# Kernel tuning notes

Hardware: AMD Instinct MI355X
Metric: run time of the kernel (lower is better)

## Reference

```python
import jax, jax.numpy as jnp
import numpy as np

EPS = 1e-12  # torch F.normalize eps


def setup_inputs() -> dict:
    key = jax.random.key(0)
    k1, k2, k3, k4, k5 = jax.random.split(key, 5)
    N, C, H, W = 32, 512, 32, 32
    E = 1024   # expansion * dim
    G = 8      # group
    D = E // G # 128, per-group channel dim
    K = 64     # num_clusters
    x = jax.random.normal(k1, (N, C, H, W), dtype=jnp.float32)
    W1 = jax.random.normal(k2, (E, C), dtype=jnp.float32) / np.sqrt(C)
    W2 = jax.random.normal(k3, (G, E), dtype=jnp.float32) / np.sqrt(E)
    Wc = jax.random.normal(k4, (K, D), dtype=jnp.float32) / np.sqrt(D)
    centroids = jax.random.uniform(k5, (K, D), dtype=jnp.float32)
    return {"x": x, "W1": W1, "W2": W2, "Wc": Wc, "centroids": centroids}


def reference(x, W1, W2, Wc, centroids):
    # x: [N, C, H, W]; W1: [E, C]; W2: [G, E]; Wc: [K, D]; centroids: [K, D]
    N, C, H, W = x.shape
    E = W1.shape[0]
    G = W2.shape[0]
    K, D = Wc.shape
    P = H * W
    # descriptor-wise L2 normalization over channel dim
    norm = jnp.linalg.norm(x, axis=1, keepdims=True)
    x = x / jnp.maximum(norm, EPS)
    # linear1 on channels: [N, E, P]
    xe = jnp.einsum('ncp,ec->nep', x.reshape(N, C, P), W1)
    # grouped features: [N, G, D, P]
    xg = xe.reshape(N, G, D, P)
    # attention gate: sigmoid(linear2)  -> [N, G, P]
    att = jax.nn.sigmoid(jnp.einsum('nep,ge->ngp', xe, W2))
    # 1x1 conv = per-pixel matmul with cluster weights -> [N, G, K, P]
    soft_assign = jax.nn.softmax(jnp.einsum('ngdp,kd->ngkp', xg, Wc), axis=2)
    # combined per-(cluster,pixel) weight
    w = soft_assign * att[:, :, None, :]  # [N, G, K, P]
    # NetVLAD residual aggregation, algebraically decomposed to avoid the
    # giant [N,G,K,D,P] intermediate:
    #   vlad[n,k,d] = sum_{g,p} w * xg  -  centroids[k,d] * sum_{g,p} w
    agg = jnp.einsum('ngkp,ngdp->nkd', w, xg)  # [N, K, D]
    wsum = w.sum(axis=(1, 3))                  # [N, K]
    vlad = agg - wsum[:, :, None] * centroids[None]  # [N, K, D]
    return vlad.reshape(N, K * D)
```

## Files before the change

kernel.cpp:

```cpp
#include <hip/hip_runtime.h>


#define N_  32
#define C_  512
#define P_  1024
#define E_  1024
#define G_  8
#define D_  128
#define K_  64

typedef __attribute__((ext_vector_type(8))) short bf16x8;
typedef __attribute__((ext_vector_type(4))) float f32x4;

__device__ __forceinline__ unsigned short f2b(float f) {
    union { float f; unsigned u; } v; v.f = f;
    unsigned r = (v.u + 0x7FFFu + ((v.u >> 16) & 1u)) >> 16;
    return (unsigned short)r;
}
__device__ __forceinline__ float b2f(unsigned short h) {
    union { unsigned u; float f; } v; v.u = ((unsigned)h) << 16;
    return v.f;
}

__device__ __forceinline__ void gl_lds16(const void* g, void* l) {
    __builtin_amdgcn_global_load_lds(
        (const __attribute__((address_space(1))) void*)g,
        (__attribute__((address_space(3))) void*)l, 16, 0, 0);
}

__global__ __launch_bounds__(256) void k0_prep(const float* __restrict__ W1,
                                               const float* __restrict__ Wc,
                                               unsigned short* __restrict__ W1b,
                                               unsigned short* __restrict__ Vb) {
    int bid = blockIdx.x;
    int t = threadIdx.x;
    int i0 = bid * 512 + t;
    W1b[i0]       = f2b(W1[i0]);
    W1b[i0 + 256] = f2b(W1[i0 + 256]);
    int ch = bid & 1, k = (bid >> 1) & 63, g = bid >> 7;
    int c = ch * 256 + t;
    float acc = 0.f;
    #pragma unroll 8
    for (int d = 0; d < 128; ++d)
        acc += Wc[k * 128 + d] * W1[(g * 128 + d) * C_ + c];
    Vb[(g * 64 + k) * C_ + c] = f2b(acc);
}

__global__ __launch_bounds__(256) void k1_norm_transpose(const float* __restrict__ x,
                                                         unsigned short* __restrict__ xhat_t) {
    __shared__ short xc[128 * 256];
    __shared__ float red[256];
    __shared__ float rn[64];
    int n = blockIdx.y;
    int p0 = blockIdx.x * 64;
    int t = threadIdx.x;
    int ps = t & 63, cs = t >> 6;

    float ss = 0.f;
    for (int i = 0; i < 128; ++i) {
        float v = x[((size_t)(n * C_ + cs * 128 + i)) * P_ + p0 + ps];
        ss += v * v;
        xc[i * 256 + t] = (short)f2b(v);
    }
    red[t] = ss;
    __syncthreads();
    if (t < 64) {
        float s = red[t] + red[64 + t] + red[128 + t] + red[192 + t];
        rn[t] = 1.0f / fmaxf(sqrtf(s), 1e-12f);
    }
    __syncthreads();

    float r = rn[ps];
    size_t base = ((size_t)(n * P_ + p0 + ps)) * C_ + cs * 128;
    #pragma unroll
    for (int jj = 0; jj < 16; ++jj) {
        bf16x8 o;
        #pragma unroll
        for (int j = 0; j < 8; ++j)
            o[j] = (short)f2b(b2f((unsigned short)xc[(jj * 8 + j) * 256 + t]) * r);
        *(bf16x8*)&xhat_t[base + jj * 8] = o;
    }
}

__global__ __launch_bounds__(256) void k2_gemm_xe(const unsigned short* __restrict__ W1b,
                                                  const unsigned short* __restrict__ xhat_t,
                                                  unsigned short* __restrict__ xe) {
    __shared__ __align__(16) short As[128 * 64];
    __shared__ __align__(16) short Bs[128 * 64];
    int n = blockIdx.y;
    int e0 = (blockIdx.x >> 3) * 128;
    int p0 = (blockIdx.x & 7) * 128;
    int t = threadIdx.x;
    int w = t >> 6, l = t & 63, q = l >> 4, l15 = l & 15;
    int wr = w >> 1, wc = w & 1;

    f32x4 acc[4][4];
    #pragma unroll
    for (int mi = 0; mi < 4; ++mi)
        #pragma unroll
        for (int ni = 0; ni < 4; ++ni)
            acc[mi][ni] = (f32x4){0.f, 0.f, 0.f, 0.f};

    for (int ks = 0; ks < 8; ++ks) {
        int k0 = ks * 64;
        #pragma unroll
        for (int i = 0; i < 4; ++i) {
            int ch = i * 256 + t;
            int row = ch >> 3, c8 = ch & 7;
            gl_lds16(&W1b[(e0 + row) * C_ + k0 + ((c8 ^ (row & 7)) * 8)], &As[ch * 8]);
        }
        #pragma unroll
        for (int i = 0; i < 4; ++i) {
            int ch = i * 256 + t;
            int row = ch >> 3, c8 = ch & 7;
            gl_lds16(&xhat_t[((size_t)(n * P_ + p0 + row)) * C_ + k0 + ((c8 ^ (row & 7)) * 8)], &Bs[ch * 8]);
        }
        __syncthreads();

        #pragma unroll
        for (int kk = 0; kk < 2; ++kk) {
            bf16x8 af[4], bf[4];
            #pragma unroll
            for (int mi = 0; mi < 4; ++mi)
                af[mi] = *(const bf16x8*)&As[(wr * 64 + mi * 16 + l15) * 64 + (((kk * 4 + q) ^ (l15 & 7)) * 8)];
            #pragma unroll
            for (int ni = 0; ni < 4; ++ni)
                bf[ni] = *(const bf16x8*)&Bs[(wc * 64 + ni * 16 + l15) * 64 + (((kk * 4 + q) ^ (l15 & 7)) * 8)];
            #pragma unroll
            for (int mi = 0; mi < 4; ++mi)
                #pragma unroll
                for (int ni = 0; ni < 4; ++ni)
                    acc[mi][ni] = __builtin_amdgcn_mfma_f32_16x16x32_bf16(af[mi], bf[ni], acc[mi][ni], 0, 0, 0);
        }
        __syncthreads();
    }

    #pragma unroll
    for (int mi = 0; mi < 4; ++mi) {
        #pragma unroll
        for (int ni = 0; ni < 4; ++ni) {
            #pragma unroll
            for (int r = 0; r < 4; ++r) {
                int e = e0 + wr * 64 + mi * 16 + q * 4 + r;
                int p = p0 + wc * 64 + ni * 16 + l15;
                xe[((size_t)(n * E_ + e)) * P_ + p] = f2b(acc[mi][ni][r]);
            }
        }
    }
}

__global__ __launch_bounds__(256) void k3a_att_part(const unsigned short* __restrict__ xe,
                                                    const float* __restrict__ W2,
                                                    float* __restrict__ att_part) {
    int n = blockIdx.y;
    int ec = blockIdx.x;
    int t = threadIdx.x;
    int e0 = ec * 64;
    f32x4 acc[8];
    #pragma unroll
    for (int g = 0; g < 8; ++g) acc[g] = (f32x4){0.f, 0.f, 0.f, 0.f};
    #pragma unroll 4
    for (int i = 0; i < 64; ++i) {
        int e = e0 + i;
        ushort4 v4 = *(const ushort4*)&xe[((size_t)(n * E_ + e)) * P_ + t * 4];
        f32x4 vf = {b2f(v4.x), b2f(v4.y), b2f(v4.z), b2f(v4.w)};
        #pragma unroll
        for (int g = 0; g < 8; ++g)
            acc[g] += vf * W2[g * E_ + e];
    }
    #pragma unroll
    for (int g = 0; g < 8; ++g)
        *(f32x4*)&att_part[(((size_t)(n * 16 + ec)) * 8 + g) * P_ + t * 4] = acc[g];
}

__global__ __launch_bounds__(256) void k3b_att_reduce(const float* __restrict__ att_part,
                                                      float* __restrict__ att_s) {
    int idx = blockIdx.x * 256 + threadIdx.x;
    int p = idx & 1023;
    int g = (idx >> 10) & 7;
    int n = idx >> 13;
    float s = 0.f;
    #pragma unroll
    for (int ec = 0; ec < 16; ++ec)
        s += att_part[(((size_t)(n * 16 + ec)) * 8 + g) * P_ + p];
    att_s[idx] = 1.0f / (1.0f + __expf(-s));
}

__global__ __launch_bounds__(256) void k4_assign_agg(const unsigned short* __restrict__ Vb,
                                                     const unsigned short* __restrict__ xhat_t,
                                                     const unsigned short* __restrict__ xe,
                                                     const float* __restrict__ att_s,
                                                     float* __restrict__ agg_part,
                                                     float* __restrict__ wsum_part) {
    __shared__ __align__(16) char smem[8192 + 16384 + 34816 + 17408];
    short* As2   = (short*)smem;
    short* Bs2   = (short*)(smem + 8192);
    short* xglds = (short*)(smem + 24576);
    short* wlds  = (short*)(smem + 59392);

    int b = blockIdx.y * 16 + blockIdx.x;
    int work = (b & 7) * 64 + (b >> 3);
    int n = work >> 4, g = work & 7, ph = (work >> 3) & 1;

    int t = threadIdx.x;
    int w = t >> 6, l = t & 63, q = l >> 4, l15 = l & 15;

    f32x4 acc_a[4][2];
    #pragma unroll
    for (int mi = 0; mi < 4; ++mi)
        #pragma unroll
        for (int ni = 0; ni < 2; ++ni)
            acc_a[mi][ni] = (f32x4){0.f, 0.f, 0.f, 0.f};
    float wsp[16];
    #pragma unroll
    for (int j = 0; j < 16; ++j) wsp[j] = 0.f;

    for (int cc = 0; cc < 4; ++cc) {
        int p0c = ph * 512 + cc * 128;

        #pragma unroll
        for (int i = 0; i < 8; ++i) {
            int ch = i * 256 + t;
            int row = ch / 17, col = (ch % 17) * 8;
            gl_lds16(&xe[((size_t)(n * E_ + g * 128 + row)) * P_ + p0c + col], &xglds[ch * 8]);
        }
        if (t < 128) {
            int ch = 2048 + t;
            int row = ch / 17, col = (ch % 17) * 8;
            gl_lds16(&xe[((size_t)(n * E_ + g * 128 + row)) * P_ + p0c + col], &xglds[ch * 8]);
        }

        f32x4 acc_s[4][2];
        #pragma unroll
        for (int mi = 0; mi < 4; ++mi)
            #pragma unroll
            for (int ni = 0; ni < 2; ++ni)
                acc_s[mi][ni] = (f32x4){0.f, 0.f, 0.f, 0.f};

        for (int ks = 0; ks < 8; ++ks) {
            int k0 = ks * 64;
            #pragma unroll
            for (int i = 0; i < 2; ++i) {
                int ch = i * 256 + t;
                int row = ch >> 3, c8 = ch & 7;
                gl_lds16(&Vb[(g * 64 + row) * C_ + k0 + ((c8 ^ (row & 7)) * 8)], &As2[ch * 8]);
            }
            #pragma unroll
            for (int i = 0; i < 4; ++i) {
                int ch = i * 256 + t;
                int row = ch >> 3, c8 = ch & 7;
                gl_lds16(&xhat_t[((size_t)(n * P_ + p0c + row)) * C_ + k0 + ((c8 ^ (row & 7)) * 8)], &Bs2[ch * 8]);
            }
            __syncthreads();
            #pragma unroll
            for (int kk = 0; kk < 2; ++kk) {
                bf16x8 af[4], bf2[2];
                #pragma unroll
                for (int mi = 0; mi < 4; ++mi)
                    af[mi] = *(const bf16x8*)&As2[(mi * 16 + l15) * 64 + (((kk * 4 + q) ^ (l15 & 7)) * 8)];
                #pragma unroll
                for (int ni = 0; ni < 2; ++ni)
                    bf2[ni] = *(const bf16x8*)&Bs2[(w * 32 + ni * 16 + l15) * 64 + (((kk * 4 + q) ^ (l15 & 7)) * 8)];
                #pragma unroll
                for (int mi = 0; mi < 4; ++mi)
                    #pragma unroll
                    for (int ni = 0; ni < 2; ++ni)
                        acc_s[mi][ni] = __builtin_amdgcn_mfma_f32_16x16x32_bf16(af[mi], bf2[ni], acc_s[mi][ni], 0, 0, 0);
            }
            __syncthreads();
        }

        #pragma unroll
        for (int ni = 0; ni < 2; ++ni) {
            float m = -1e30f;
            #pragma unroll
            for (int mi = 0; mi < 4; ++mi)
                #pragma unroll
                for (int r = 0; r < 4; ++r)
                    m = fmaxf(m, acc_s[mi][ni][r]);
            m = fmaxf(m, __shfl_xor(m, 16));
            m = fmaxf(m, __shfl_xor(m, 32));
            float s = 0.f;
            #pragma unroll
            for (int mi = 0; mi < 4; ++mi)
                #pragma unroll
                for (int r = 0; r < 4; ++r) {
                    float e = __expf(acc_s[mi][ni][r] - m);
                    acc_s[mi][ni][r] = e;
                    s += e;
                }
            s += __shfl_xor(s, 16);
            s += __shfl_xor(s, 32);

            int pcol = p0c + w * 32 + ni * 16 + l15;
            float av = att_s[(((size_t)(n * G_ + g)) * P_) + pcol];
            float scale = av / s;

            #pragma unroll
            for (int mi = 0; mi < 4; ++mi)
                #pragma unroll
                for (int r = 0; r < 4; ++r) {
                    float wv = acc_s[mi][ni][r] * scale;
                    wsp[mi * 4 + r] += wv;
                    wlds[(mi * 16 + q * 4 + r) * 136 + (w * 32 + ni * 16 + l15)] = (short)f2b(wv);
                }
        }
        __syncthreads();

        #pragma unroll
        for (int pk = 0; pk < 4; ++pk) {
            bf16x8 a2[4], b2[2];
            #pragma unroll
            for (int mi = 0; mi < 4; ++mi)
                a2[mi] = *(const bf16x8*)&wlds[(mi * 16 + l15) * 136 + pk * 32 + q * 8];
            #pragma unroll
            for (int ni = 0; ni < 2; ++ni)
                b2[ni] = *(const bf16x8*)&xglds[(w * 32 + ni * 16 + l15) * 136 + pk * 32 + q * 8];
            #pragma unroll
            for (int mi = 0; mi < 4; ++mi)
                #pragma unroll
                for (int ni = 0; ni < 2; ++ni)
                    acc_a[mi][ni] = __builtin_amdgcn_mfma_f32_16x16x32_bf16(a2[mi], b2[ni], acc_a[mi][ni], 0, 0, 0);
        }
        __syncthreads();
    }

    size_t base = (((size_t)(n * G_ + g)) * 2 + ph) * 64;
    #pragma unroll
    for (int mi = 0; mi < 4; ++mi)
        #pragma unroll
        for (int ni = 0; ni < 2; ++ni)
            #pragma unroll
            for (int r = 0; r < 4; ++r) {
                int k = mi * 16 + q * 4 + r;
                int d = w * 32 + ni * 16 + l15;
                agg_part[(base + k) * 128 + d] = acc_a[mi][ni][r];
            }

    #pragma unroll
    for (int j = 0; j < 16; ++j) {
        float v = wsp[j];
        v += __shfl_xor(v, 1);
        v += __shfl_xor(v, 2);
        v += __shfl_xor(v, 4);
        v += __shfl_xor(v, 8);
        if (l15 == 0) {
            int k = (j >> 2) * 16 + q * 4 + (j & 3);
            wsum_part[((((size_t)(n * G_ + g)) * 2 + ph) * 4 + w) * 64 + k] = v;
        }
    }
}

__global__ __launch_bounds__(256) void k5_final(const float* __restrict__ agg_part,
                                                const float* __restrict__ wsum_part,
                                                const float* __restrict__ centroids,
                                                float* __restrict__ out) {
    int idx = blockIdx.x * 256 + threadIdx.x;
    int d = idx & 127;
    int k = (idx >> 7) & 63;
    int n = idx >> 13;
    float ws = 0.f;
    #pragma unroll
    for (int g = 0; g < 8; ++g)
        #pragma unroll
        for (int ph = 0; ph < 2; ++ph)
            #pragma unroll
            for (int w2 = 0; w2 < 4; ++w2)
                ws += wsum_part[((((size_t)(n * G_ + g)) * 2 + ph) * 4 + w2) * 64 + k];
    float agg = 0.f;
    #pragma unroll
    for (int g = 0; g < 8; ++g)
        #pragma unroll
        for (int ph = 0; ph < 2; ++ph)
            agg += agg_part[(((((size_t)(n * G_ + g)) * 2 + ph) * 64) + k) * 128 + d];
    out[idx] = agg - ws * centroids[k * 128 + d];
}

extern "C" void kernel_launch(void* const* d_in, const int* in_sizes, int n_in,
                              void* d_out, int out_size, void* d_ws, size_t ws_size,
                              hipStream_t stream) {
    const float* x         = (const float*)d_in[0];
    const float* W1        = (const float*)d_in[1];
    const float* W2        = (const float*)d_in[2];
    const float* Wc        = (const float*)d_in[3];
    const float* centroids = (const float*)d_in[4];
    float* out = (float*)d_out;

    char* ws = (char*)d_ws;
    unsigned short* W1b      = (unsigned short*)(ws + 0);
    unsigned short* Vb       = (unsigned short*)(ws + 1048576);
    unsigned short* xhat_t   = (unsigned short*)(ws + 1572864);
    unsigned short* xe       = (unsigned short*)(ws + 35127296);
    float*          att_s    = (float*)(ws + 102236160);
    float*          att_part = (float*)(ws + 103284736);
    float*          agg_part = (float*)(ws + 103284736);
    float*          wsum_part= (float*)(ws + 120061952);

    hipLaunchKernelGGL(k0_prep,        dim3(1024), dim3(256), 0, stream, W1, Wc, W1b, Vb);
    hipLaunchKernelGGL(k1_norm_transpose, dim3(16, 32), dim3(256), 0, stream, x, xhat_t);
    hipLaunchKernelGGL(k2_gemm_xe,     dim3(64, 32), dim3(256), 0, stream, W1b, xhat_t, xe);
    hipLaunchKernelGGL(k3a_att_part,   dim3(16, 32), dim3(256), 0, stream, xe, W2, att_part);
    hipLaunchKernelGGL(k3b_att_reduce, dim3(1024), dim3(256), 0, stream, att_part, att_s);
    hipLaunchKernelGGL(k4_assign_agg,  dim3(16, 32), dim3(256), 0, stream, Vb, xhat_t, xe,
                       att_s, agg_part, wsum_part);
    hipLaunchKernelGGL(k5_final,       dim3(1024), dim3(256), 0, stream,
                       agg_part, wsum_part, centroids, out);
}
```

Measured before the change: 242.7 us.

## Double-buffer assignment GEMM in k4 with register A-fragments and manual waitcnt pipeline

Rewrites the k4 soft-assignment GEMM loop as a fully unrolled double-buffered pipeline. The xhat tiles alternate between two LDS buffers, the Vb fragments are loaded straight into registers instead of staged through LDS, and explicit vmcnt waits with sched barriers overlap the next loads with the current MFMAs. The xg tile load moves to the end of the pipeline and uses an XOR-swizzled 128-wide layout instead of padding, and the LDS for the w tile now aliases the B buffers. The attention values are prefetched early. The hand-set waitcnt counts and buffer aliasing are fragile and raise register pressure.

```diff
diff --git a/kernel.cpp b/kernel.cpp
--- a/kernel.cpp
+++ b/kernel.cpp
@@ -27,6 +27,9 @@
         (const __attribute__((address_space(1))) void*)g,
         (__attribute__((address_space(3))) void*)l, 16, 0, 0);
 }
+
+#define SB  __builtin_amdgcn_sched_barrier(0)
+#define BAR __builtin_amdgcn_s_barrier()
 
 __global__ __launch_bounds__(256) void k0_prep(const float* __restrict__ W1,
                                                const float* __restrict__ Wc,
@@ -186,17 +189,67 @@
     att_s[idx] = 1.0f / (1.0f + __expf(-s));
 }
 
+__device__ __forceinline__ void load_af(bf16x8* dst, const unsigned short* __restrict__ Vb,
+                                        int g, int ks, int l15, int q) {
+    #pragma unroll
+    for (int mi = 0; mi < 4; ++mi)
+        #pragma unroll
+        for (int kk = 0; kk < 2; ++kk)
+            dst[mi * 2 + kk] = *(const bf16x8*)&Vb[(size_t)((g * 64 + mi * 16 + l15) * C_)
+                                                  + ks * 64 + kk * 32 + q * 8];
+}
+
+__device__ __forceinline__ void stage_b(short* buf, const unsigned short* __restrict__ xhat_t,
+                                        int n, int p0c, int k0, int t) {
+    #pragma unroll
+    for (int i = 0; i < 4; ++i) {
+        int ch = i * 256 + t;
+        int row = ch >> 3, c8 = ch & 7;
+        gl_lds16(&xhat_t[((size_t)(n * P_ + p0c + row)) * C_ + k0 + ((c8 ^ (row & 7)) * 8)],
+                 &buf[ch * 8]);
+    }
+}
+
+__device__ __forceinline__ void stage_xg(short* xglds, const unsigned short* __restrict__ xe,
+                                         int n, int g, int p0c, int t) {
+    #pragma unroll
+    for (int i = 0; i < 8; ++i) {
+        int ch = i * 256 + t;
+        int row = ch >> 4, c16 = ch & 15;
+        gl_lds16(&xe[((size_t)(n * E_ + g * 128 + row)) * P_ + p0c + ((c16 ^ (row & 7)) * 8)],
+                 &xglds[ch * 8]);
+    }
+}
+
+__device__ __forceinline__ void mfma_s(f32x4 acc[4][2], const short* buf, const bf16x8* af,
+                                       int w, int q, int l15) {
+    #pragma unroll
+    for (int kk = 0; kk < 2; ++kk) {
+        bf16x8 b[2];
+        #pragma unroll
+        for (int ni = 0; ni < 2; ++ni)
+            b[ni] = *(const bf16x8*)&buf[(w * 32 + ni * 16 + l15) * 64
+                                         + (((kk * 4 + q) ^ (l15 & 7)) * 8)];
+        #pragma unroll
+        for (int mi = 0; mi < 4; ++mi)
+            #pragma unroll
+            for (int ni = 0; ni < 2; ++ni)
+                acc[mi][ni] = __builtin_amdgcn_mfma_f32_16x16x32_bf16(
+                    af[mi * 2 + kk], b[ni], acc[mi][ni], 0, 0, 0);
+    }
+}
+
 __global__ __launch_bounds__(256) void k4_assign_agg(const unsigned short* __restrict__ Vb,
                                                      const unsigned short* __restrict__ xhat_t,
                                                      const unsigned short* __restrict__ xe,
                                                      const float* __restrict__ att_s,
                                                      float* __restrict__ agg_part,
                                                      float* __restrict__ wsum_part) {
-    __shared__ __align__(16) char smem[8192 + 16384 + 34816 + 17408];
-    short* As2   = (short*)smem;
-    short* Bs2   = (short*)(smem + 8192);
-    short* xglds = (short*)(smem + 24576);
-    short* wlds  = (short*)(smem + 59392);
+    __shared__ __align__(16) char smem[65536];
+    short* Bs0   = (short*)smem;
+    short* Bs1   = (short*)(smem + 16384);
+    short* xglds = (short*)(smem + 32768);
+    short* wlds  = (short*)smem;
 
     int b = blockIdx.y * 16 + blockIdx.x;
     int work = (b & 7) * 64 + (b >> 3);
@@ -215,21 +268,10 @@
     #pragma unroll
     for (int j = 0; j < 16; ++j) wsp[j] = 0.f;
 
+    #pragma unroll 1
     for (int cc = 0; cc < 4; ++cc) {
         int p0c = ph * 512 + cc * 128;
 
-        #pragma unroll
-        for (int i = 0; i < 8; ++i) {
-            int ch = i * 256 + t;
-            int row = ch / 17, col = (ch % 17) * 8;
-            gl_lds16(&xe[((size_t)(n * E_ + g * 128 + row)) * P_ + p0c + col], &xglds[ch * 8]);
-        }
-        if (t < 128) {
-            int ch = 2048 + t;
-            int row = ch / 17, col = (ch % 17) * 8;
-            gl_lds16(&xe[((size_t)(n * E_ + g * 128 + row)) * P_ + p0c + col], &xglds[ch * 8]);
-        }
-
         f32x4 acc_s[4][2];
         #pragma unroll
         for (int mi = 0; mi < 4; ++mi)
@@ -237,38 +279,45 @@
             for (int ni = 0; ni < 2; ++ni)
                 acc_s[mi][ni] = (f32x4){0.f, 0.f, 0.f, 0.f};
 
-        for (int ks = 0; ks < 8; ++ks) {
-            int k0 = ks * 64;
-            #pragma unroll
-            for (int i = 0; i < 2; ++i) {
-                int ch = i * 256 + t;
-                int row = ch >> 3, c8 = ch & 7;
-                gl_lds16(&Vb[(g * 64 + row) * C_ + k0 + ((c8 ^ (row & 7)) * 8)], &As2[ch * 8]);
-            }
-            #pragma unroll
-            for (int i = 0; i < 4; ++i) {
-                int ch = i * 256 + t;
-                int row = ch >> 3, c8 = ch & 7;
-                gl_lds16(&xhat_t[((size_t)(n * P_ + p0c + row)) * C_ + k0 + ((c8 ^ (row & 7)) * 8)], &Bs2[ch * 8]);
-            }
-            __syncthreads();
-            #pragma unroll
-            for (int kk = 0; kk < 2; ++kk) {
-                bf16x8 af[4], bf2[2];
-                #pragma unroll
-                for (int mi = 0; mi < 4; ++mi)
-                    af[mi] = *(const bf16x8*)&As2[(mi * 16 + l15) * 64 + (((kk * 4 + q) ^ (l15 & 7)) * 8)];
-                #pragma unroll
-                for (int ni = 0; ni < 2; ++ni)
-                    bf2[ni] = *(const bf16x8*)&Bs2[(w * 32 + ni * 16 + l15) * 64 + (((kk * 4 + q) ^ (l15 & 7)) * 8)];
-                #pragma unroll
-                for (int mi = 0; mi < 4; ++mi)
-                    #pragma unroll
-                    for (int ni = 0; ni < 2; ++ni)
-                        acc_s[mi][ni] = __builtin_amdgcn_mfma_f32_16x16x32_bf16(af[mi], bf2[ni], acc_s[mi][ni], 0, 0, 0);
-            }
-            __syncthreads();
-        }
+        bf16x8 afA[8], afB[8];
+
+        stage_b(Bs0, xhat_t, n, p0c, 0, t); SB;
+        load_af(afA, Vb, g, 0, l15, q); SB;
+        float av0 = att_s[(size_t)(n * G_ + g) * P_ + p0c + w * 32 + l15];
+        float av1 = att_s[(size_t)(n * G_ + g) * P_ + p0c + w * 32 + 16 + l15];
+        SB;
+
+        load_af(afB, Vb, g, 1, l15, q); SB;
+        stage_b(Bs1, xhat_t, n, p0c, 64, t); SB;
+        asm volatile("s_waitcnt vmcnt(12)" ::: "memory"); SB; BAR; SB;
+        mfma_s(acc_s, Bs0, afA, w, q, l15); SB; BAR; SB;
+        load_af(afA, Vb, g, 2, l15, q); SB;
+        stage_b(Bs0, xhat_t, n, p0c, 128, t); SB;
+        asm volatile("s_waitcnt vmcnt(12)" ::: "memory"); SB; BAR; SB;
+        mfma_s(acc_s, Bs1, afB, w, q, l15); SB; BAR; SB;
+        load_af(afB, Vb, g, 3, l15, q); SB;
+        stage_b(Bs1, xhat_t, n, p0c, 192, t); SB;
+        asm volatile("s_waitcnt vmcnt(12)" ::: "memory"); SB; BAR; SB;
+        mfma_s(acc_s, Bs0, afA, w, q, l15); SB; BAR; SB;
+        load_af(afA, Vb, g, 4, l15, q); SB;
+        stage_b(Bs0, xhat_t, n, p0c, 256, t); SB;
+        asm volatile("s_waitcnt vmcnt(12)" ::: "memory"); SB; BAR; SB;
+        mfma_s(acc_s, Bs1, afB, w, q, l15); SB; BAR; SB;
+        load_af(afB, Vb, g, 5, l15, q); SB;
+        stage_b(Bs1, xhat_t, n, p0c, 320, t); SB;
+        asm volatile("s_waitcnt vmcnt(12)" ::: "memory"); SB; BAR; SB;
+        mfma_s(acc_s, Bs0, afA, w, q, l15); SB; BAR; SB;
+        load_af(afA, Vb, g, 6, l15, q); SB;
+        stage_b(Bs0, xhat_t, n, p0c, 384, t); SB;
+        asm volatile("s_waitcnt vmcnt(12)" ::: "memory"); SB; BAR; SB;
+        mfma_s(acc_s, Bs1, afB, w, q, l15); SB; BAR; SB;
+        load_af(afB, Vb, g, 7, l15, q); SB;
+        stage_b(Bs1, xhat_t, n, p0c, 448, t); SB;
+        stage_xg(xglds, xe, n, g, p0c, t); SB;
+        asm volatile("s_waitcnt vmcnt(20)" ::: "memory"); SB; BAR; SB;
+        mfma_s(acc_s, Bs0, afA, w, q, l15); SB; BAR; SB;
+        asm volatile("s_waitcnt vmcnt(8)" ::: "memory"); SB; BAR; SB;
+        mfma_s(acc_s, Bs1, afB, w, q, l15); SB; BAR; SB;
 
         #pragma unroll
         for (int ni = 0; ni < 2; ++ni) {
@@ -292,8 +341,7 @@
             s += __shfl_xor(s, 16);
             s += __shfl_xor(s, 32);
 
-            int pcol = p0c + w * 32 + ni * 16 + l15;
-            float av = att_s[(((size_t)(n * G_ + g)) * P_) + pcol];
+            float av = ni ? av1 : av0;
             float scale = av / s;
 
             #pragma unroll
@@ -315,7 +363,8 @@
                 a2[mi] = *(const bf16x8*)&wlds[(mi * 16 + l15) * 136 + pk * 32 + q * 8];
             #pragma unroll
             for (int ni = 0; ni < 2; ++ni)
-                b2[ni] = *(const bf16x8*)&xglds[(w * 32 + ni * 16 + l15) * 136 + pk * 32 + q * 8];
+                b2[ni] = *(const bf16x8*)&xglds[(w * 32 + ni * 16 + l15) * 128
+                                                + (((pk * 4 + q) ^ (l15 & 7)) * 8)];
             #pragma unroll
             for (int mi = 0; mi < 4; ++mi)
                 #pragma unroll
```

New measurement: 279.4 us. 1.15x slower.

## Widen assign-agg kernel to 512 threads with aliased LDS and in-block wsum reduction

Applied to the files above, without the earlier changes.

The assignment/aggregation kernel now runs with 8 waves per block instead of 4. Each wave handles 16 pixels in the soft-assign GEMM and a 32x32 (k,d) tile in the aggregation GEMM, which halves per-thread accumulators. The xe tile is stored unpadded with an XOR swizzle, and the weight buffer is aliased onto the A/B staging region, so LDS per block shrinks. The per-wave wsum partials are reduced inside the block, which lets the final kernel read 4x fewer partials. This aims at more resident waves and better latency hiding, at the cost of extra barriers and more blocks competing for LDS.

```diff
diff --git a/kernel.cpp b/kernel.cpp
--- a/kernel.cpp
+++ b/kernel.cpp
@@ -186,17 +186,18 @@
     att_s[idx] = 1.0f / (1.0f + __expf(-s));
 }
 
-__global__ __launch_bounds__(256) void k4_assign_agg(const unsigned short* __restrict__ Vb,
-                                                     const unsigned short* __restrict__ xhat_t,
-                                                     const unsigned short* __restrict__ xe,
-                                                     const float* __restrict__ att_s,
-                                                     float* __restrict__ agg_part,
-                                                     float* __restrict__ wsum_part) {
-    __shared__ __align__(16) char smem[8192 + 16384 + 34816 + 17408];
+__global__ __launch_bounds__(512, 4) void k4_assign_agg(const unsigned short* __restrict__ Vb,
+                                                        const unsigned short* __restrict__ xhat_t,
+                                                        const unsigned short* __restrict__ xe,
+                                                        const float* __restrict__ att_s,
+                                                        float* __restrict__ agg_part,
+                                                        float* __restrict__ wsum_part) {
+    __shared__ __align__(16) char smem[8192 + 16384 + 32768];
     short* As2   = (short*)smem;
     short* Bs2   = (short*)(smem + 8192);
     short* xglds = (short*)(smem + 24576);
-    short* wlds  = (short*)(smem + 59392);
+    short* wlds  = (short*)smem;
+    float* wred  = (float*)smem;
 
     int b = blockIdx.y * 16 + blockIdx.x;
     int work = (b & 7) * 64 + (b >> 3);
@@ -204,10 +205,11 @@
 
     int t = threadIdx.x;
     int w = t >> 6, l = t & 63, q = l >> 4, l15 = l & 15;
-
-    f32x4 acc_a[4][2];
-    #pragma unroll
-    for (int mi = 0; mi < 4; ++mi)
+    int kh = w >> 2, dq = w & 3;
+
+    f32x4 acc_a[2][2];
+    #pragma unroll
+    for (int mi = 0; mi < 2; ++mi)
         #pragma unroll
         for (int ni = 0; ni < 2; ++ni)
             acc_a[mi][ni] = (f32x4){0.f, 0.f, 0.f, 0.f};
@@ -219,65 +221,52 @@
         int p0c = ph * 512 + cc * 128;
 
         #pragma unroll
-        for (int i = 0; i < 8; ++i) {
-            int ch = i * 256 + t;
-            int row = ch / 17, col = (ch % 17) * 8;
-            gl_lds16(&xe[((size_t)(n * E_ + g * 128 + row)) * P_ + p0c + col], &xglds[ch * 8]);
-        }
-        if (t < 128) {
-            int ch = 2048 + t;
-            int row = ch / 17, col = (ch % 17) * 8;
-            gl_lds16(&xe[((size_t)(n * E_ + g * 128 + row)) * P_ + p0c + col], &xglds[ch * 8]);
-        }
-
-        f32x4 acc_s[4][2];
+        for (int i = 0; i < 4; ++i) {
+            int ch = i * 512 + t;
+            int row = ch >> 4, c16 = ch & 15;
+            gl_lds16(&xe[((size_t)(n * E_ + g * 128 + row)) * P_ + p0c + ((c16 ^ (row & 7)) * 8)],
+                     &xglds[ch * 8]);
+        }
+
+        f32x4 acc_s[4];
         #pragma unroll
         for (int mi = 0; mi < 4; ++mi)
-            #pragma unroll
-            for (int ni = 0; ni < 2; ++ni)
-                acc_s[mi][ni] = (f32x4){0.f, 0.f, 0.f, 0.f};
+            acc_s[mi] = (f32x4){0.f, 0.f, 0.f, 0.f};
 
         for (int ks = 0; ks < 8; ++ks) {
             int k0 = ks * 64;
+            {
+                int row = t >> 3, c8 = t & 7;
+                gl_lds16(&Vb[(g * 64 + row) * C_ + k0 + ((c8 ^ (row & 7)) * 8)], &As2[t * 8]);
+            }
             #pragma unroll
             for (int i = 0; i < 2; ++i) {
-                int ch = i * 256 + t;
-                int row = ch >> 3, c8 = ch & 7;
-                gl_lds16(&Vb[(g * 64 + row) * C_ + k0 + ((c8 ^ (row & 7)) * 8)], &As2[ch * 8]);
-            }
-            #pragma unroll
-            for (int i = 0; i < 4; ++i) {
-                int ch = i * 256 + t;
+                int ch = i * 512 + t;
                 int row = ch >> 3, c8 = ch & 7;
                 gl_lds16(&xhat_t[((size_t)(n * P_ + p0c + row)) * C_ + k0 + ((c8 ^ (row & 7)) * 8)], &Bs2[ch * 8]);
             }
             __syncthreads();
             #pragma unroll
             for (int kk = 0; kk < 2; ++kk) {
-                bf16x8 af[4], bf2[2];
+                bf16x8 af[4], bfr;
                 #pragma unroll
                 for (int mi = 0; mi < 4; ++mi)
                     af[mi] = *(const bf16x8*)&As2[(mi * 16 + l15) * 64 + (((kk * 4 + q) ^ (l15 & 7)) * 8)];
-                #pragma unroll
-                for (int ni = 0; ni < 2; ++ni)
-                    bf2[ni] = *(const bf16x8*)&Bs2[(w * 32 + ni * 16 + l15) * 64 + (((kk * 4 + q) ^ (l15 & 7)) * 8)];
+                bfr = *(const bf16x8*)&Bs2[(w * 16 + l15) * 64 + (((kk * 4 + q) ^ (l15 & 7)) * 8)];
                 #pragma unroll
                 for (int mi = 0; mi < 4; ++mi)
-                    #pragma unroll
-                    for (int ni = 0; ni < 2; ++ni)
-                        acc_s[mi][ni] = __builtin_amdgcn_mfma_f32_16x16x32_bf16(af[mi], bf2[ni], acc_s[mi][ni], 0, 0, 0);
+                    acc_s[mi] = __builtin_amdgcn_mfma_f32_16x16x32_bf16(af[mi], bfr, acc_s[mi], 0, 0, 0);
             }
             __syncthreads();
         }
 
-        #pragma unroll
-        for (int ni = 0; ni < 2; ++ni) {
+        {
             float m = -1e30f;
             #pragma unroll
             for (int mi = 0; mi < 4; ++mi)
                 #pragma unroll
                 for (int r = 0; r < 4; ++r)
-                    m = fmaxf(m, acc_s[mi][ni][r]);
+                    m = fmaxf(m, acc_s[mi][r]);
             m = fmaxf(m, __shfl_xor(m, 16));
             m = fmaxf(m, __shfl_xor(m, 32));
             float s = 0.f;
@@ -285,39 +274,39 @@
             for (int mi = 0; mi < 4; ++mi)
                 #pragma unroll
                 for (int r = 0; r < 4; ++r) {
-                    float e = __expf(acc_s[mi][ni][r] - m);
-                    acc_s[mi][ni][r] = e;
+                    float e = __expf(acc_s[mi][r] - m);
+                    acc_s[mi][r] = e;
                     s += e;
                 }
             s += __shfl_xor(s, 16);
             s += __shfl_xor(s, 32);
 
-            int pcol = p0c + w * 32 + ni * 16 + l15;
-            float av = att_s[(((size_t)(n * G_ + g)) * P_) + pcol];
+            float av = att_s[(((size_t)(n * G_ + g)) * P_) + p0c + w * 16 + l15];
             float scale = av / s;
 
             #pragma unroll
             for (int mi = 0; mi < 4; ++mi)
                 #pragma unroll
                 for (int r = 0; r < 4; ++r) {
-                    float wv = acc_s[mi][ni][r] * scale;
+                    float wv = acc_s[mi][r] * scale;
                     wsp[mi * 4 + r] += wv;
-                    wlds[(mi * 16 + q * 4 + r) * 136 + (w * 32 + ni * 16 + l15)] = (short)f2b(wv);
+                    wlds[(mi * 16 + q * 4 + r) * 136 + (w * 16 + l15)] = (short)f2b(wv);
                 }
         }
         __syncthreads();
 
         #pragma unroll
         for (int pk = 0; pk < 4; ++pk) {
-            bf16x8 a2[4], b2[2];
-            #pragma unroll
-            for (int mi = 0; mi < 4; ++mi)
-                a2[mi] = *(const bf16x8*)&wlds[(mi * 16 + l15) * 136 + pk * 32 + q * 8];
+            bf16x8 a2[2], b2[2];
+            #pragma unroll
+            for (int mi = 0; mi < 2; ++mi)
+                a2[mi] = *(const bf16x8*)&wlds[(kh * 32 + mi * 16 + l15) * 136 + pk * 32 + q * 8];
             #pragma unroll
             for (int ni = 0; ni < 2; ++ni)
-                b2[ni] = *(const bf16x8*)&xglds[(w * 32 + ni * 16 + l15) * 136 + pk * 32 + q * 8];
-            #pragma unroll
-            for (int mi = 0; mi < 4; ++mi)
+                b2[ni] = *(const bf16x8*)&xglds[(dq * 32 + ni * 16 + l15) * 128
+                                                + (((pk * 4 + q) ^ (l15 & 7)) * 8)];
+            #pragma unroll
+            for (int mi = 0; mi < 2; ++mi)
                 #pragma unroll
                 for (int ni = 0; ni < 2; ++ni)
                     acc_a[mi][ni] = __builtin_amdgcn_mfma_f32_16x16x32_bf16(a2[mi], b2[ni], acc_a[mi][ni], 0, 0, 0);
@@ -327,13 +316,13 @@
 
     size_t base = (((size_t)(n * G_ + g)) * 2 + ph) * 64;
     #pragma unroll
-    for (int mi = 0; mi < 4; ++mi)
+    for (int mi = 0; mi < 2; ++mi)
         #pragma unroll
         for (int ni = 0; ni < 2; ++ni)
             #pragma unroll
             for (int r = 0; r < 4; ++r) {
-                int k = mi * 16 + q * 4 + r;
-                int d = w * 32 + ni * 16 + l15;
+                int k = kh * 32 + mi * 16 + q * 4 + r;
+                int d = dq * 32 + ni * 16 + l15;
                 agg_part[(base + k) * 128 + d] = acc_a[mi][ni][r];
             }
 
@@ -346,8 +335,16 @@
         v += __shfl_xor(v, 8);
         if (l15 == 0) {
             int k = (j >> 2) * 16 + q * 4 + (j & 3);
-            wsum_part[((((size_t)(n * G_ + g)) * 2 + ph) * 4 + w) * 64 + k] = v;
-        }
+            wred[w * 64 + k] = v;
+        }
+    }
+    __syncthreads();
+    if (t < 64) {
+        float s = 0.f;
+        #pragma unroll
+        for (int wv = 0; wv < 8; ++wv)
+            s += wred[wv * 64 + t];
+        wsum_part[(((size_t)(n * G_ + g)) * 2 + ph) * 64 + t] = s;
     }
 }
 
@@ -364,9 +361,7 @@
     for (int g = 0; g < 8; ++g)
         #pragma unroll
         for (int ph = 0; ph < 2; ++ph)
-            #pragma unroll
-            for (int w2 = 0; w2 < 4; ++w2)
-                ws += wsum_part[((((size_t)(n * G_ + g)) * 2 + ph) * 4 + w2) * 64 + k];
+            ws += wsum_part[(((size_t)(n * G_ + g)) * 2 + ph) * 64 + k];
     float agg = 0.f;
     #pragma unroll
     for (int g = 0; g < 8; ++g)
@@ -401,7 +396,7 @@
     hipLaunchKernelGGL(k2_gemm_xe,     dim3(64, 32), dim3(256), 0, stream, W1b, xhat_t, xe);
     hipLaunchKernelGGL(k3a_att_part,   dim3(16, 32), dim3(256), 0, stream, xe, W2, att_part);
     hipLaunchKernelGGL(k3b_att_reduce, dim3(1024), dim3(256), 0, stream, att_part, att_s);
-    hipLaunchKernelGGL(k4_assign_agg,  dim3(16, 32), dim3(256), 0, stream, Vb, xhat_t, xe,
+    hipLaunchKernelGGL(k4_assign_agg,  dim3(16, 32), dim3(512), 0, stream, Vb, xhat_t, xe,
                        att_s, agg_part, wsum_part);
     hipLaunchKernelGGL(k5_final,       dim3(1024), dim3(256), 0, stream,
                        agg_part, wsum_part, centroids, out);
```

After: 233.3 us. -3.9%, faster.
